# Kernel optimization log

Measured on AMD Instinct MI355X. Metric: run time of the kernel, lower is better.

The kernel has to match this reference:

```python
import jax, jax.numpy as jnp
import numpy as np

B, N, CIN, CK, M0 = 2, 4096, 64, 64, 64
NS = 16  # nsample; split into NS//2 cosine + NS//2 euclidean neighbors
LEAKY = 0.1


def _leaky(x):
    return jax.nn.leaky_relu(x, LEAKY)


def _knn_cosine(k, xyz, new_xyz):
    # xyz [B,M,C], new_xyz [B,S,C] -> idx [B,S,k] of smallest cosine distance
    s = new_xyz / jnp.sqrt(jnp.sum(new_xyz ** 2, -1, keepdims=True) + 1e-8)
    d = xyz / jnp.sqrt(jnp.sum(xyz ** 2, -1, keepdims=True) + 1e-8)
    dist = 1.0 - jnp.einsum('bsc,bmc->bsm', s, d)
    return jax.lax.top_k(-dist, k)[1]


def _knn_euclid(k, xyz, new_xyz):
    # squared euclidean distance [B,S,M]
    dist = (jnp.sum(new_xyz ** 2, -1)[:, :, None]
            + jnp.sum(xyz ** 2, -1)[:, None, :]
            - 2.0 * jnp.einsum('bsc,bmc->bsm', new_xyz, xyz))
    return jax.lax.top_k(-dist, k)[1]


def _group(points, idx):
    # points [B,M,C], idx [B,S,K] -> [B,S,K,C]
    return jax.vmap(lambda p, i: p[i])(points, idx)


def _cross(xyz1, xyz2, p1, p2, k1, k2, W_pos, b_pos, W_m1, b_m1, W_m2, b_m2):
    # all point tensors channel-first [B,C,N]; transpose to [B,N,C]
    xyz1t = xyz1.transpose(0, 2, 1)
    xyz2t = xyz2.transpose(0, 2, 1)
    p1t = p1.transpose(0, 2, 1)
    p2t = p2.transpose(0, 2, 1)
    k1t = k1.transpose(0, 2, 1)
    k2t = k2.transpose(0, 2, 1)
    kh = NS // 2
    idx_c = _knn_cosine(kh, k2t, k1t)      # [B,N1,kh] feature-space KNN
    idx_p = _knn_euclid(kh, xyz2t, xyz1t)  # [B,N1,kh] xyz-space KNN
    neighbor_xyz = jnp.concatenate([_group(xyz2t, idx_c), _group(xyz2t, idx_p)], axis=2)  # [B,N1,NS,3]
    direction = neighbor_xyz - xyz1t[:, :, None, :]
    g2 = jnp.concatenate([_group(p2t, idx_c), _group(p2t, idx_p)], axis=2)  # [B,N1,NS,D]
    pos = jnp.einsum('bnkc,dc->bnkd', direction, W_pos) + b_pos  # 1x1 conv on xyz offsets
    new = _leaky(g2 + p1t[:, :, None, :] + pos)  # fused add + leaky relu (bn=Identity)
    new = _leaky(jnp.einsum('bnkd,ed->bnke', new, W_m1) + b_m1)
    new = _leaky(jnp.einsum('bnkd,ed->bnke', new, W_m2) + b_m2)
    new = jnp.max(new, axis=2)  # max-pool over neighbor dim -> [B,N1,D]
    return new.transpose(0, 2, 1)  # [B,D,N1]


def setup_inputs() -> dict:
    key = jax.random.key(0)
    ks = jax.random.split(key, 12)
    rn = lambda k, shape, s=1.0: jax.random.normal(k, shape, jnp.float32) * s
    return {
        'pc1': rn(ks[0], (B, 3, N)),
        'pc2': rn(ks[1], (B, 3, N)),
        'feat1': rn(ks[2], (B, CIN, N)),
        'feat2': rn(ks[3], (B, CIN, N)),
        'knn1': rn(ks[4], (B, CK, N)),
        'knn2': rn(ks[5], (B, CK, N)),
        'W_t11': rn(ks[6], (M0, CIN), 0.1),
        'b_t11': jnp.zeros((M0,), jnp.float32),
        'W_t22': rn(ks[7], (M0, CIN), 0.1),
        'b_t22': jnp.zeros((M0,), jnp.float32),
        'W_pos': rn(ks[8], (M0, 3), 0.1),
        'b_pos': jnp.zeros((M0,), jnp.float32),
        'W_m1': rn(ks[9], (M0, M0), 0.1),
        'b_m1': jnp.zeros((M0,), jnp.float32),
        'W_m2': rn(ks[10], (M0, M0), 0.1),
        'b_m2': jnp.zeros((M0,), jnp.float32),
    }


def reference(pc1, pc2, feat1, feat2, knn1, knn2,
              W_t11, b_t11, W_t22, b_t22, W_pos, b_pos,
              W_m1, b_m1, W_m2, b_m2):
    # cross_t11 / cross_t22: 1x1 Conv1d in_channel -> mlp[0]
    f1a = jnp.einsum('dc,bcn->bdn', W_t11, feat1) + b_t11[None, :, None]
    f2a = jnp.einsum('dc,bcn->bdn', W_t22, feat2) + b_t22[None, :, None]
    f2b = jnp.einsum('dc,bcn->bdn', W_t11, feat2) + b_t11[None, :, None]
    f1b = jnp.einsum('dc,bcn->bdn', W_t22, feat1) + b_t22[None, :, None]
    feat1_new = _cross(pc1, pc2, f1a, f2a, knn1, knn2, W_pos, b_pos, W_m1, b_m1, W_m2, b_m2)
    feat2_new = _cross(pc2, pc1, f2b, f1b, knn2, knn1, W_pos, b_pos, W_m1, b_m1, W_m2, b_m2)
    return (feat1_new, feat2_new)
```

## Files before the change

### kernel.cpp

```cpp
#include <hip/hip_runtime.h>
#include <hip/hip_bf16.h>

#define BB 2
#define NN 4096
#define CH 64

typedef __bf16 bf16x8 __attribute__((ext_vector_type(8)));
typedef float f32x4 __attribute__((ext_vector_type(4)));

__device__ __forceinline__ float lrelu(float v) { return fmaxf(v, 0.1f * v); }
__device__ __forceinline__ float tobf(const __hip_bfloat16& h) { return __bfloat162float(h); }

#define PC1_C 0
#define PC2_C 24576
#define F1_C 49152
#define F2_C 573440
#define K1_C 1097728
#define K2_C 1622016
#define WT11_C 2146304
#define BT11_C 2150400
#define WT22_C 2150464
#define BT22_C 2154560
#define WPOS_C 2154624
#define BPOS_C 2154816
#define WM1_C 2154880
#define BM1_C 2158976
#define WM2_C 2159040
#define BM2_C 2163136
#define CN_TOTAL 2163200

__device__ __forceinline__ unsigned fmap(float s) {
  unsigned u = __float_as_uint(s);
  return u ^ ((unsigned)((int)u >> 31) | 0x80000000u);
}

__device__ __forceinline__ unsigned umaxu(unsigned a, unsigned b) { return a > b ? a : b; }
__device__ __forceinline__ void casu(unsigned& a, unsigned& b) {
  unsigned mx = a > b ? a : b;
  unsigned mn = a > b ? b : a;
  a = mx; b = mn;
}

__device__ __forceinline__ void bitonic8(unsigned bd[8]) {
  casu(bd[0], bd[4]); casu(bd[1], bd[5]); casu(bd[2], bd[6]); casu(bd[3], bd[7]);
  casu(bd[0], bd[2]); casu(bd[1], bd[3]); casu(bd[4], bd[6]); casu(bd[5], bd[7]);
  casu(bd[0], bd[1]); casu(bd[2], bd[3]); casu(bd[4], bd[5]); casu(bd[6], bd[7]);
}

__device__ __forceinline__ void merge4(unsigned bd[8], unsigned k0, unsigned k1,
                                       unsigned k2, unsigned k3) {
  casu(k0, k1); casu(k2, k3); casu(k0, k2); casu(k1, k3); casu(k1, k2);
  bd[4] = umaxu(bd[4], k3); bd[5] = umaxu(bd[5], k2);
  bd[6] = umaxu(bd[6], k1); bd[7] = umaxu(bd[7], k0);
  bitonic8(bd);
}

__device__ __forceinline__ void merge88(unsigned a[8], const unsigned b[8]) {
  a[0] = umaxu(a[0], b[7]); a[1] = umaxu(a[1], b[6]);
  a[2] = umaxu(a[2], b[5]); a[3] = umaxu(a[3], b[4]);
  a[4] = umaxu(a[4], b[3]); a[5] = umaxu(a[5], b[2]);
  a[6] = umaxu(a[6], b[1]); a[7] = umaxu(a[7], b[0]);
  bitonic8(a);
}

__global__ void k_detect(const unsigned short* __restrict__ pc1raw, int* __restrict__ flag) {
  int lane = threadIdx.x;
  int bad = 0;
#pragma unroll
  for (int i = 0; i < 64; ++i) {
    unsigned short u = pc1raw[lane * 64 + i];
    int e = (u >> 7) & 0xFF;
    bad += (e >= 140) ? 1 : 0;
  }
#pragma unroll
  for (int s = 32; s; s >>= 1) bad += __shfl_xor(bad, s, 64);
  if (lane == 0) *flag = (bad > 16) ? 1 : 0;
}

__global__ __launch_bounds__(256) void k_ingest(
    const void* p0, const void* p1, const void* p2, const void* p3,
    const void* p4, const void* p5, const void* p6, const void* p7,
    const void* p8, const void* p9, const void* p10, const void* p11,
    const void* p12, const void* p13, const void* p14, const void* p15,
    const int* __restrict__ flag, float* __restrict__ dst) {
  const int cum[17] = {0, 24576, 49152, 573440, 1097728, 1622016, 2146304, 2150400,
                       2150464, 2154560, 2154624, 2154816, 2154880, 2158976, 2159040,
                       2163136, 2163200};
  size_t t = (size_t)blockIdx.x * 256 + threadIdx.x;
  if (t >= (size_t)CN_TOTAL) return;
  int seg = 0;
#pragma unroll
  for (int i = 1; i < 16; ++i) seg += (t >= (size_t)cum[i]) ? 1 : 0;
  size_t local = t - (size_t)cum[seg];
  const void* ptrs[16] = {p0, p1, p2, p3, p4, p5, p6, p7, p8, p9, p10, p11, p12, p13, p14, p15};
  const void* p = ptrs[seg];
  float v;
  if (*flag) v = ((const float*)p)[local];
  else       v = tobf(((const __hip_bfloat16*)p)[local]);
  if (!(v == v) || fabsf(v) > 1e30f) v = 0.f;
  dst[t] = v;
}

__global__ __launch_bounds__(256) void k_prep_misc(const float* __restrict__ cn,
                                                   __hip_bfloat16* __restrict__ wmb,
                                                   float4* __restrict__ xyzt,
                                                   float4* __restrict__ wp4) {
  int bid = blockIdx.x;
  if (bid < 32) {
    int t = bid * 256 + threadIdx.x;
    float v = (t < 4096) ? cn[WM1_C + t] : cn[WM2_C + (t - 4096)];
    wmb[t] = __float2bfloat16(v);
  } else if (bid < 96) {
    int t = (bid - 32) * 256 + threadIdx.x;
    int n = t & (NN - 1);
    int b = (t >> 12) & 1;
    int a = t >> 13;
    const float* p = cn + (a ? PC2_C : PC1_C) + (size_t)b * 3 * NN + n;
    float x = p[0], y = p[NN], z = p[2 * NN];
    xyzt[(size_t)(a * BB + b) * NN + n] = make_float4(x, y, z, x * x + y * y + z * z);
  } else {
    int c = threadIdx.x;
    if (c < 64)
      wp4[c] = make_float4(cn[WPOS_C + 3 * c], cn[WPOS_C + 3 * c + 1],
                           cn[WPOS_C + 3 * c + 2], cn[BPOS_C + c]);
  }
}

__global__ __launch_bounds__(256) void k_prep_knn(const float* __restrict__ cn,
                                                  float* __restrict__ knnt,
                                                  __hip_bfloat16* __restrict__ knnb) {
  int t = blockIdx.x * 256 + threadIdx.x;
  int n = t & (NN - 1);
  int b = (t >> 12) & 1;
  int a = t >> 13;
  const float* col = cn + (a ? K2_C : K1_C) + (size_t)b * CH * NN + n;
  float s = 0.f;
#pragma unroll
  for (int c = 0; c < CH; ++c) { float v = col[(size_t)c * NN]; s += v * v; }
  float inv = 1.0f / sqrtf(s + 1e-8f);
  size_t row = (size_t)(a * BB + b) * NN + n;
  float* o = knnt + row * CH;
  __hip_bfloat16* ob = knnb + row * CH;
#pragma unroll
  for (int c = 0; c < CH; ++c) {
    float v = col[(size_t)c * NN] * inv;
    o[c] = v;
    ob[c] = __float2bfloat16(v);
  }
}

__global__ __launch_bounds__(256) void k_conv(const float* __restrict__ cn,
                                              float* __restrict__ fbuf) {
  __shared__ float wl[CH * CH];
  int bid = blockIdx.x;
  int tile = bid & (NN / 4 - 1);
  int b = (bid >> 10) & 1;
  int sel = bid >> 11;
  const float* W = cn + ((sel == 0 || sel == 2) ? WT11_C : WT22_C);
  const float* bias = cn + ((sel == 0 || sel == 2) ? BT11_C : BT22_C);
  const float* feat = cn + ((sel == 0 || sel == 3) ? F1_C : F2_C);
  int t = threadIdx.x;
#pragma unroll
  for (int i = 0; i < 16; ++i) {
    int e = t * 16 + i;
    wl[(e & 63) * 64 + (e >> 6)] = W[e];
  }
  __syncthreads();
  int p = t >> 6, d = t & 63;
  int n = tile * 4 + p;
  const float* fc = feat + (size_t)b * CH * NN + n;
  float acc = bias[d];
#pragma unroll
  for (int c = 0; c < CH; ++c) acc += wl[c * 64 + d] * fc[(size_t)c * NN];
  fbuf[((size_t)(sel * BB + b) * NN + n) * CH + d] = acc;
}

__global__ __launch_bounds__(512, 4) void k_knn3(const __hip_bfloat16* __restrict__ knnb,
                                                 const float* __restrict__ knnt,
                                                 const float4* __restrict__ xyzt,
                                                 int* __restrict__ idxf) {
  __shared__ unsigned skc[16 * 8 * 33];
  __shared__ unsigned ske[16 * 8 * 33];
  __shared__ int cidx[16 * 16];
  int bid = blockIdx.x;
  int qt = bid & (NN / 16 - 1);
  int b = (bid >> 8) & 1;
  int x = bid >> 9;
  int w = threadIdx.x >> 6;
  int lane = threadIdx.x & 63;
  int lo = lane & 15, g = lane >> 4;
  int q0 = qt * 16;
  int j0 = w * (NN / 8);
  int ss = w * 4 + g;
  int hw = lane >> 5, sl = lane & 31;
  int qq = w * 2 + hw;
  size_t qbase = (size_t)(x * BB + b) * NN;
  size_t dbase = (size_t)((1 - x) * BB + b) * NN;

  const __hip_bfloat16* qb = knnb + (qbase + q0) * CH;
  bf16x8 qf0 = *reinterpret_cast<const bf16x8*>(qb + lo * CH + g * 8);
  bf16x8 qf1 = *reinterpret_cast<const bf16x8*>(qb + lo * CH + 32 + g * 8);
  const __hip_bfloat16* db = knnb + dbase * CH;
  const float4 q4 = xyzt[qbase + q0 + lo];
  const float4* dbx = xyzt + dbase;
  float tx = 2.f * q4.x, ty = 2.f * q4.y, tz = 2.f * q4.z;

  unsigned bc0[8], bc1[8], be0[8], be1[8];
#pragma unroll
  for (int k = 0; k < 8; ++k) { bc0[k] = 0u; bc1[k] = 0u; be0[k] = 0u; be1[k] = 0u; }

  auto TILE = [&](unsigned (&bc)[8], unsigned (&be)[8], int jb) {
    unsigned rc = (unsigned)(4095 - jb - g * 4);
    const __hip_bfloat16* ar = db + (size_t)(jb + lo) * CH + g * 8;
    bf16x8 a0 = *reinterpret_cast<const bf16x8*>(ar);
    bf16x8 a1 = *reinterpret_cast<const bf16x8*>(ar + 32);
    f32x4 acc = {0.f, 0.f, 0.f, 0.f};
    acc = __builtin_amdgcn_mfma_f32_16x16x32_bf16(a0, qf0, acc, 0, 0, 0);
    acc = __builtin_amdgcn_mfma_f32_16x16x32_bf16(a1, qf1, acc, 0, 0, 0);
    int je = jb + g * 4;
    float4 p0 = dbx[je], p1 = dbx[je + 1], p2 = dbx[je + 2], p3 = dbx[je + 3];
    float v0 = fmaf(tx, p0.x, fmaf(ty, p0.y, fmaf(tz, p0.z, -p0.w)));
    float v1 = fmaf(tx, p1.x, fmaf(ty, p1.y, fmaf(tz, p1.z, -p1.w)));
    float v2 = fmaf(tx, p2.x, fmaf(ty, p2.y, fmaf(tz, p2.z, -p2.w)));
    float v3 = fmaf(tx, p3.x, fmaf(ty, p3.y, fmaf(tz, p3.z, -p3.w)));
    merge4(bc, (__float_as_uint(acc[0] + 4.0f) & 0xFFFFF000u) | rc,
               (__float_as_uint(acc[1] + 4.0f) & 0xFFFFF000u) | (rc - 1),
               (__float_as_uint(acc[2] + 4.0f) & 0xFFFFF000u) | (rc - 2),
               (__float_as_uint(acc[3] + 4.0f) & 0xFFFFF000u) | (rc - 3));
    merge4(be, (fmap(v0) & 0xFFFFF000u) | rc,
               (fmap(v1) & 0xFFFFF000u) | (rc - 1),
               (fmap(v2) & 0xFFFFF000u) | (rc - 2),
               (fmap(v3) & 0xFFFFF000u) | (rc - 3));
  };

  for (int t = 0; t < 16; ++t) {
    TILE(bc0, be0, j0 + (2 * t) * 16);
    TILE(bc1, be1, j0 + (2 * t + 1) * 16);
  }
  merge88(bc0, bc1);
  merge88(be0, be1);
#pragma unroll
  for (int k = 0; k < 8; ++k) {
    skc[(lo * 8 + k) * 33 + ss] = bc0[k];
    ske[(lo * 8 + k) * 33 + ss] = be0[k];
  }
  __syncthreads();

  {
    unsigned e[16];
#pragma unroll
    for (int k = 0; k < 8; ++k) e[k] = skc[(qq * 8 + k) * 33 + sl];
#pragma unroll
    for (int k = 8; k < 16; ++k) e[k] = 0u;
#pragma unroll
    for (int s = 1; s < 32; s <<= 1) {
      unsigned f[16];
#pragma unroll
      for (int k = 0; k < 16; ++k) f[k] = (unsigned)__shfl_xor((int)e[k], s, 64);
#pragma unroll
      for (int i = 0; i < 16; ++i) e[i] = umaxu(e[i], f[15 - i]);
      casu(e[0], e[8]); casu(e[1], e[9]); casu(e[2], e[10]); casu(e[3], e[11]);
      casu(e[4], e[12]); casu(e[5], e[13]); casu(e[6], e[14]); casu(e[7], e[15]);
      casu(e[0], e[4]); casu(e[1], e[5]); casu(e[2], e[6]); casu(e[3], e[7]);
      casu(e[8], e[12]); casu(e[9], e[13]); casu(e[10], e[14]); casu(e[11], e[15]);
      casu(e[0], e[2]); casu(e[1], e[3]); casu(e[4], e[6]); casu(e[5], e[7]);
      casu(e[8], e[10]); casu(e[9], e[11]); casu(e[12], e[14]); casu(e[13], e[15]);
      casu(e[0], e[1]); casu(e[2], e[3]); casu(e[4], e[5]); casu(e[6], e[7]);
      casu(e[8], e[9]); casu(e[10], e[11]); casu(e[12], e[13]); casu(e[14], e[15]);
    }
    if (sl == 0) {
#pragma unroll
      for (int k = 0; k < 16; ++k) cidx[qq * 16 + k] = 4095 - (int)(e[k] & 4095u);
    }
    int c = sl >> 1, hr = sl & 1;
    int idx = cidx[qq * 16 + c];
    const float4* qr = reinterpret_cast<const float4*>(knnt + (qbase + q0 + qq) * CH) + hr * 8;
    const float4* dr = reinterpret_cast<const float4*>(knnt + (dbase + idx) * CH) + hr * 8;
    float v = 0.f;
#pragma unroll 4
    for (int cb = 0; cb < 8; ++cb) {
      float4 qv = qr[cb], dv = dr[cb];
      v += qv.x * dv.x + qv.y * dv.y + qv.z * dv.z + qv.w * dv.w;
    }
    v += __shfl_xor(v, 1, 64);
    float cv = v; int ci = idx; int wsel = 0;
#pragma unroll
    for (int k = 0; k < 8; ++k) {
      float av = cv; int ai = ci;
#pragma unroll
      for (int s = 1; s < 32; s <<= 1) {
        float ov = __shfl_xor(av, s, 64);
        int oi = __shfl_xor(ai, s, 64);
        bool bt = (ov > av) || (ov == av && oi < ai);
        av = bt ? ov : av; ai = bt ? oi : ai;
      }
      if (sl == k) wsel = ai;
      if (ci == ai) cv = -1e38f;
    }
    if (sl < 8) idxf[(qbase + q0 + qq) * 16 + sl] = wsel;
  }

  {
    unsigned e[16];
#pragma unroll
    for (int k = 0; k < 8; ++k) e[k] = ske[(qq * 8 + k) * 33 + sl];
#pragma unroll
    for (int k = 8; k < 16; ++k) e[k] = 0u;
#pragma unroll
    for (int s = 1; s < 32; s <<= 1) {
      unsigned f[16];
#pragma unroll
      for (int k = 0; k < 16; ++k) f[k] = (unsigned)__shfl_xor((int)e[k], s, 64);
#pragma unroll
      for (int i = 0; i < 16; ++i) e[i] = umaxu(e[i], f[15 - i]);
      casu(e[0], e[8]); casu(e[1], e[9]); casu(e[2], e[10]); casu(e[3], e[11]);
      casu(e[4], e[12]); casu(e[5], e[13]); casu(e[6], e[14]); casu(e[7], e[15]);
      casu(e[0], e[4]); casu(e[1], e[5]); casu(e[2], e[6]); casu(e[3], e[7]);
      casu(e[8], e[12]); casu(e[9], e[13]); casu(e[10], e[14]); casu(e[11], e[15]);
      casu(e[0], e[2]); casu(e[1], e[3]); casu(e[4], e[6]); casu(e[5], e[7]);
      casu(e[8], e[10]); casu(e[9], e[11]); casu(e[12], e[14]); casu(e[13], e[15]);
      casu(e[0], e[1]); casu(e[2], e[3]); casu(e[4], e[5]); casu(e[6], e[7]);
      casu(e[8], e[9]); casu(e[10], e[11]); casu(e[12], e[13]); casu(e[14], e[15]);
    }
    if (sl == 0) {
#pragma unroll
      for (int k = 0; k < 16; ++k) cidx[qq * 16 + k] = 4095 - (int)(e[k] & 4095u);
    }
    int c = sl >> 1;
    int idx = cidx[qq * 16 + c];
    const float4 qx4 = xyzt[qbase + q0 + qq];
    float4 p = xyzt[dbase + idx];
    float v = fmaf(2.f * qx4.x, p.x, fmaf(2.f * qx4.y, p.y, fmaf(2.f * qx4.z, p.z, -p.w)));
    float cv = v; int ci = idx; int wsel = 0;
#pragma unroll
    for (int k = 0; k < 8; ++k) {
      float av = cv; int ai = ci;
#pragma unroll
      for (int s = 1; s < 32; s <<= 1) {
        float ov = __shfl_xor(av, s, 64);
        int oi = __shfl_xor(ai, s, 64);
        bool bt = (ov > av) || (ov == av && oi < ai);
        av = bt ? ov : av; ai = bt ? oi : ai;
      }
      if (sl == k) wsel = ai;
      if (ci == ai) cv = -1e38f;
    }
    if (sl < 8) idxf[(qbase + q0 + qq) * 16 + 8 + sl] = wsel;
  }
}

__global__ __launch_bounds__(256) void k_mlp(const float* __restrict__ fbuf,
                                             const float4* __restrict__ xyzt,
                                             const int* __restrict__ idxf,
                                             const float4* __restrict__ wp4,
                                             const __hip_bfloat16* __restrict__ wmb,
                                             const float* __restrict__ cn,
                                             float* __restrict__ out) {
  __shared__ __bf16 h1s[4 * 16 * 72];
  const int t = threadIdx.x;
  const int wv = t >> 6, L = t & 63;
  const int lo = L & 15, g = L >> 4;
  int bid = blockIdx.x;
  const int qt = bid & (NN / 4 - 1);
  const int b = (bid >> 10) & 1;
  const int x = bid >> 11;
  const int q = qt * 4 + wv;

  bf16x8 w1f[4][2], w2f[4][2];
#pragma unroll
  for (int tt = 0; tt < 4; ++tt)
#pragma unroll
    for (int kc = 0; kc < 2; ++kc) {
      int e = tt * 16 + lo, c0 = kc * 32 + g * 8;
      w1f[tt][kc] = *reinterpret_cast<const bf16x8*>(wmb + e * 64 + c0);
      w2f[tt][kc] = *reinterpret_cast<const bf16x8*>(wmb + 4096 + e * 64 + c0);
    }

  const float* pq  = fbuf + ((size_t)((x ? 2 : 0) * BB + b)) * NN * CH;
  const float* pdb = fbuf + ((size_t)((x ? 3 : 1) * BB + b)) * NN * CH;
  const float4* qx  = xyzt + (size_t)(x * BB + b) * NN;
  const float4* dbx = xyzt + (size_t)((1 - x) * BB + b) * NN;

  const int m = lo;
  int jm = idxf[(((size_t)x * BB + b) * NN + q) * 16 + m];
  jm &= (NN - 1);
  const float4 q4 = qx[q];
  const float4 p4 = dbx[jm];
  const float dx = p4.x - q4.x, dy = p4.y - q4.y, dz = p4.z - q4.z;

  const float4* g2v = reinterpret_cast<const float4*>(pdb + (size_t)jm * CH);
  const float4* pqv = reinterpret_cast<const float4*>(pq + (size_t)q * CH);
  float hv[16];
  {
    float4 t0 = g2v[g * 2], t1 = g2v[g * 2 + 1], t2 = g2v[g * 2 + 8], t3 = g2v[g * 2 + 9];
    float4 u0 = pqv[g * 2], u1 = pqv[g * 2 + 1], u2 = pqv[g * 2 + 8], u3 = pqv[g * 2 + 9];
    hv[0] = t0.x + u0.x; hv[1] = t0.y + u0.y; hv[2] = t0.z + u0.z; hv[3] = t0.w + u0.w;
    hv[4] = t1.x + u1.x; hv[5] = t1.y + u1.y; hv[6] = t1.z + u1.z; hv[7] = t1.w + u1.w;
    hv[8] = t2.x + u2.x; hv[9] = t2.y + u2.y; hv[10] = t2.z + u2.z; hv[11] = t2.w + u2.w;
    hv[12] = t3.x + u3.x; hv[13] = t3.y + u3.y; hv[14] = t3.z + u3.z; hv[15] = t3.w + u3.w;
  }

  bf16x8 a0, a1;
#pragma unroll
  for (int kc = 0; kc < 2; ++kc) {
#pragma unroll
    for (int j = 0; j < 8; ++j) {
      int c = kc * 32 + g * 8 + j;
      float4 wp = wp4[c];
      float v = hv[kc * 8 + j] + wp.x * dx + wp.y * dy + wp.z * dz + wp.w;
      v = lrelu(v);
      if (kc == 0) a0[j] = (__bf16)v; else a1[j] = (__bf16)v;
    }
  }

  __bf16* hrow = h1s + wv * 16 * 72;
#pragma unroll
  for (int tt = 0; tt < 4; ++tt) {
    float bv = cn[BM1_C + tt * 16 + lo];
    f32x4 acc = {bv, bv, bv, bv};
    acc = __builtin_amdgcn_mfma_f32_16x16x32_bf16(a0, w1f[tt][0], acc, 0, 0, 0);
    acc = __builtin_amdgcn_mfma_f32_16x16x32_bf16(a1, w1f[tt][1], acc, 0, 0, 0);
#pragma unroll
    for (int r = 0; r < 4; ++r) {
      float v = lrelu(acc[r]);
      hrow[(g * 4 + r) * 72 + tt * 16 + lo] = (__bf16)v;
    }
  }
  __syncthreads();
  bf16x8 h1a = *reinterpret_cast<const bf16x8*>(hrow + m * 72 + g * 8);
  bf16x8 h1b = *reinterpret_cast<const bf16x8*>(hrow + m * 72 + 32 + g * 8);

  size_t obase = ((size_t)(x * BB + b) * CH) * NN;
#pragma unroll
  for (int tt = 0; tt < 4; ++tt) {
    float bv = cn[BM2_C + tt * 16 + lo];
    f32x4 acc = {bv, bv, bv, bv};
    acc = __builtin_amdgcn_mfma_f32_16x16x32_bf16(h1a, w2f[tt][0], acc, 0, 0, 0);
    acc = __builtin_amdgcn_mfma_f32_16x16x32_bf16(h1b, w2f[tt][1], acc, 0, 0, 0);
    float v = fmaxf(fmaxf(lrelu(acc[0]), lrelu(acc[1])), fmaxf(lrelu(acc[2]), lrelu(acc[3])));
    v = fmaxf(v, __shfl_xor(v, 16, 64));
    v = fmaxf(v, __shfl_xor(v, 32, 64));
    if (g == 0) out[obase + (size_t)(tt * 16 + lo) * NN + q] = v;
  }
}

#define CN_OFF 0
#define FB_OFF ((size_t)CN_TOTAL)
#define KT_OFF (FB_OFF + (size_t)4 * BB * NN * CH)
#define XZ_OFF (KT_OFF + (size_t)2 * BB * NN * CH)
#define WP4_OFF (XZ_OFF + (size_t)2 * BB * NN * 4)
#define WMB_OFF (WP4_OFF + 256)
#define IDX_OFF (WMB_OFF + 4096)
#define FLAG_OFF (IDX_OFF + 262144)
#define KNB_OFF (FLAG_OFF + 4)

extern "C" void kernel_launch(void* const* d_in, const int* in_sizes, int n_in,
                              void* d_out, int out_size, void* d_ws, size_t ws_size,
                              hipStream_t stream) {
  float* ws = (float*)d_ws;
  float* cn = ws + CN_OFF;
  int* flag = (int*)(ws + FLAG_OFF);

  k_detect<<<1, 64, 0, stream>>>((const unsigned short*)d_in[0], flag);
  k_ingest<<<(CN_TOTAL + 255) / 256, 256, 0, stream>>>(
      d_in[0], d_in[1], d_in[2], d_in[3], d_in[4], d_in[5], d_in[6], d_in[7],
      d_in[8], d_in[9], d_in[10], d_in[11], d_in[12], d_in[13], d_in[14], d_in[15],
      flag, cn);
  k_prep_misc<<<97, 256, 0, stream>>>(cn, (__hip_bfloat16*)(ws + WMB_OFF),
                                      (float4*)(ws + XZ_OFF), (float4*)(ws + WP4_OFF));
  k_prep_knn<<<(2 * BB * NN) / 256, 256, 0, stream>>>(cn, ws + KT_OFF,
                                                     (__hip_bfloat16*)(ws + KNB_OFF));
  k_conv<<<4 * BB * (NN / 4), 256, 0, stream>>>(cn, ws + FB_OFF);
  k_knn3<<<2 * BB * (NN / 16), 512, 0, stream>>>(
      (const __hip_bfloat16*)(ws + KNB_OFF), ws + KT_OFF,
      (const float4*)(ws + XZ_OFF), (int*)(ws + IDX_OFF));
  k_mlp<<<2 * BB * (NN / 4), 256, 0, stream>>>(ws + FB_OFF, (const float4*)(ws + XZ_OFF),
                                               (const int*)(ws + IDX_OFF), (const float4*)(ws + WP4_OFF),
                                               (const __hip_bfloat16*)(ws + WMB_OFF), cn,
                                               (float*)d_out);
}
```

Baseline: 311.7 us.

## Prefetch KNN tiles, share one LDS buffer, use bitonic sort for rerank

The KNN kernel's main loop now software-pipelines its loads, issuing the bf16 feature and xyz loads for the next tile before the MFMA and merge work on the current tile. The cosine and euclidean candidate exchanges share a single LDS buffer with an extra barrier between them, halving that shared memory to help occupancy. The exact-distance refinement swaps eight serial argmax reductions for a bitonic sort across the 32 lanes. Risks include higher register pressure from holding two tiles of loads at once, and a change in tie-break order if the bitonic network differs from the old selection.

```diff
diff --git a/kernel.cpp b/kernel.cpp
--- a/kernel.cpp
+++ b/kernel.cpp
@@ -175,12 +175,11 @@
   fbuf[((size_t)(sel * BB + b) * NN + n) * CH + d] = acc;
 }
 
-__global__ __launch_bounds__(512, 4) void k_knn3(const __hip_bfloat16* __restrict__ knnb,
+__global__ __launch_bounds__(512, 4) void k_knn4(const __hip_bfloat16* __restrict__ knnb,
                                                  const float* __restrict__ knnt,
                                                  const float4* __restrict__ xyzt,
                                                  int* __restrict__ idxf) {
-  __shared__ unsigned skc[16 * 8 * 33];
-  __shared__ unsigned ske[16 * 8 * 33];
+  __shared__ unsigned sk[16 * 8 * 33];
   __shared__ int cidx[16 * 16];
   int bid = blockIdx.x;
   int qt = bid & (NN / 16 - 1);
@@ -209,47 +208,67 @@
 #pragma unroll
   for (int k = 0; k < 8; ++k) { bc0[k] = 0u; bc1[k] = 0u; be0[k] = 0u; be1[k] = 0u; }
 
-  auto TILE = [&](unsigned (&bc)[8], unsigned (&be)[8], int jb) {
-    unsigned rc = (unsigned)(4095 - jb - g * 4);
-    const __hip_bfloat16* ar = db + (size_t)(jb + lo) * CH + g * 8;
-    bf16x8 a0 = *reinterpret_cast<const bf16x8*>(ar);
-    bf16x8 a1 = *reinterpret_cast<const bf16x8*>(ar + 32);
+  auto STEP = [&](const bf16x8& A0, const bf16x8& A1, const float4& P0,
+                  const float4& P1, const float4& P2, const float4& P3,
+                  int rcv, unsigned (&bc)[8], unsigned (&be)[8]) {
     f32x4 acc = {0.f, 0.f, 0.f, 0.f};
-    acc = __builtin_amdgcn_mfma_f32_16x16x32_bf16(a0, qf0, acc, 0, 0, 0);
-    acc = __builtin_amdgcn_mfma_f32_16x16x32_bf16(a1, qf1, acc, 0, 0, 0);
-    int je = jb + g * 4;
-    float4 p0 = dbx[je], p1 = dbx[je + 1], p2 = dbx[je + 2], p3 = dbx[je + 3];
-    float v0 = fmaf(tx, p0.x, fmaf(ty, p0.y, fmaf(tz, p0.z, -p0.w)));
-    float v1 = fmaf(tx, p1.x, fmaf(ty, p1.y, fmaf(tz, p1.z, -p1.w)));
-    float v2 = fmaf(tx, p2.x, fmaf(ty, p2.y, fmaf(tz, p2.z, -p2.w)));
-    float v3 = fmaf(tx, p3.x, fmaf(ty, p3.y, fmaf(tz, p3.z, -p3.w)));
-    merge4(bc, (__float_as_uint(acc[0] + 4.0f) & 0xFFFFF000u) | rc,
-               (__float_as_uint(acc[1] + 4.0f) & 0xFFFFF000u) | (rc - 1),
-               (__float_as_uint(acc[2] + 4.0f) & 0xFFFFF000u) | (rc - 2),
-               (__float_as_uint(acc[3] + 4.0f) & 0xFFFFF000u) | (rc - 3));
-    merge4(be, (fmap(v0) & 0xFFFFF000u) | rc,
-               (fmap(v1) & 0xFFFFF000u) | (rc - 1),
-               (fmap(v2) & 0xFFFFF000u) | (rc - 2),
-               (fmap(v3) & 0xFFFFF000u) | (rc - 3));
+    acc = __builtin_amdgcn_mfma_f32_16x16x32_bf16(A0, qf0, acc, 0, 0, 0);
+    acc = __builtin_amdgcn_mfma_f32_16x16x32_bf16(A1, qf1, acc, 0, 0, 0);
+    float v0 = fmaf(tx, P0.x, fmaf(ty, P0.y, fmaf(tz, P0.z, -P0.w)));
+    float v1 = fmaf(tx, P1.x, fmaf(ty, P1.y, fmaf(tz, P1.z, -P1.w)));
+    float v2 = fmaf(tx, P2.x, fmaf(ty, P2.y, fmaf(tz, P2.z, -P2.w)));
+    float v3 = fmaf(tx, P3.x, fmaf(ty, P3.y, fmaf(tz, P3.z, -P3.w)));
+    unsigned r = (unsigned)rcv;
+    merge4(bc, (__float_as_uint(acc[0] + 4.0f) & 0xFFFFF000u) | r,
+               (__float_as_uint(acc[1] + 4.0f) & 0xFFFFF000u) | (r - 1),
+               (__float_as_uint(acc[2] + 4.0f) & 0xFFFFF000u) | (r - 2),
+               (__float_as_uint(acc[3] + 4.0f) & 0xFFFFF000u) | (r - 3));
+    merge4(be, (fmap(v0) & 0xFFFFF000u) | r,
+               (fmap(v1) & 0xFFFFF000u) | (r - 1),
+               (fmap(v2) & 0xFFFFF000u) | (r - 2),
+               (fmap(v3) & 0xFFFFF000u) | (r - 3));
   };
 
-  for (int t = 0; t < 16; ++t) {
-    TILE(bc0, be0, j0 + (2 * t) * 16);
-    TILE(bc1, be1, j0 + (2 * t + 1) * 16);
+  const __hip_bfloat16* arA = db + (size_t)(j0 + lo) * CH + g * 8;
+  const __hip_bfloat16* arB = arA + 16 * CH;
+  const float4* peA = dbx + j0 + g * 4;
+  const float4* peB = peA + 16;
+  int rc = 4095 - j0 - g * 4;
+
+  bf16x8 aA0 = *reinterpret_cast<const bf16x8*>(arA);
+  bf16x8 aA1 = *reinterpret_cast<const bf16x8*>(arA + 32);
+  float4 pA0 = peA[0], pA1 = peA[1], pA2 = peA[2], pA3 = peA[3];
+
+  for (int i = 0; i < 15; ++i) {
+    bf16x8 aB0 = *reinterpret_cast<const bf16x8*>(arB);
+    bf16x8 aB1 = *reinterpret_cast<const bf16x8*>(arB + 32);
+    float4 pB0 = peB[0], pB1 = peB[1], pB2 = peB[2], pB3 = peB[3];
+    STEP(aA0, aA1, pA0, pA1, pA2, pA3, rc, bc0, be0);
+    arA += 32 * CH; peA += 32;
+    aA0 = *reinterpret_cast<const bf16x8*>(arA);
+    aA1 = *reinterpret_cast<const bf16x8*>(arA + 32);
+    pA0 = peA[0]; pA1 = peA[1]; pA2 = peA[2]; pA3 = peA[3];
+    STEP(aB0, aB1, pB0, pB1, pB2, pB3, rc - 16, bc1, be1);
+    arB += 32 * CH; peB += 32;
+    rc -= 32;
+  }
+  {
+    bf16x8 aB0 = *reinterpret_cast<const bf16x8*>(arB);
+    bf16x8 aB1 = *reinterpret_cast<const bf16x8*>(arB + 32);
+    float4 pB0 = peB[0], pB1 = peB[1], pB2 = peB[2], pB3 = peB[3];
+    STEP(aA0, aA1, pA0, pA1, pA2, pA3, rc, bc0, be0);
+    STEP(aB0, aB1, pB0, pB1, pB2, pB3, rc - 16, bc1, be1);
   }
   merge88(bc0, bc1);
   merge88(be0, be1);
-#pragma unroll
-  for (int k = 0; k < 8; ++k) {
-    skc[(lo * 8 + k) * 33 + ss] = bc0[k];
-    ske[(lo * 8 + k) * 33 + ss] = be0[k];
-  }
+
+#pragma unroll
+  for (int k = 0; k < 8; ++k) sk[(lo * 8 + k) * 33 + ss] = bc0[k];
   __syncthreads();
-
   {
     unsigned e[16];
 #pragma unroll
-    for (int k = 0; k < 8; ++k) e[k] = skc[(qq * 8 + k) * 33 + sl];
+    for (int k = 0; k < 8; ++k) e[k] = sk[(qq * 8 + k) * 33 + sl];
 #pragma unroll
     for (int k = 8; k < 16; ++k) e[k] = 0u;
 #pragma unroll
@@ -283,27 +302,31 @@
       v += qv.x * dv.x + qv.y * dv.y + qv.z * dv.z + qv.w * dv.w;
     }
     v += __shfl_xor(v, 1, 64);
-    float cv = v; int ci = idx; int wsel = 0;
-#pragma unroll
-    for (int k = 0; k < 8; ++k) {
-      float av = cv; int ai = ci;
-#pragma unroll
-      for (int s = 1; s < 32; s <<= 1) {
-        float ov = __shfl_xor(av, s, 64);
-        int oi = __shfl_xor(ai, s, 64);
-        bool bt = (ov > av) || (ov == av && oi < ai);
-        av = bt ? ov : av; ai = bt ? oi : ai;
+    int ii = idx;
+#pragma unroll
+    for (int k = 2; k <= 32; k <<= 1) {
+#pragma unroll
+      for (int j = k >> 1; j >= 1; j >>= 1) {
+        float ov = __shfl_xor(v, j, 64);
+        int oi = __shfl_xor(ii, j, 64);
+        bool ob = (ov > v) || (ov == v && oi < ii);
+        bool want = (((sl & k) == 0) == ((sl & j) == 0));
+        bool take = (want == ob);
+        v = take ? ov : v;
+        ii = take ? oi : ii;
       }
-      if (sl == k) wsel = ai;
-      if (ci == ai) cv = -1e38f;
-    }
-    if (sl < 8) idxf[(qbase + q0 + qq) * 16 + sl] = wsel;
-  }
-
+    }
+    if (sl < 16 && (sl & 1) == 0) idxf[(qbase + q0 + qq) * 16 + (sl >> 1)] = ii;
+  }
+  __syncthreads();
+
+#pragma unroll
+  for (int k = 0; k < 8; ++k) sk[(lo * 8 + k) * 33 + ss] = be0[k];
+  __syncthreads();
   {
     unsigned e[16];
 #pragma unroll
-    for (int k = 0; k < 8; ++k) e[k] = ske[(qq * 8 + k) * 33 + sl];
+    for (int k = 0; k < 8; ++k) e[k] = sk[(qq * 8 + k) * 33 + sl];
 #pragma unroll
     for (int k = 8; k < 16; ++k) e[k] = 0u;
 #pragma unroll
@@ -331,21 +354,21 @@
     const float4 qx4 = xyzt[qbase + q0 + qq];
     float4 p = xyzt[dbase + idx];
     float v = fmaf(2.f * qx4.x, p.x, fmaf(2.f * qx4.y, p.y, fmaf(2.f * qx4.z, p.z, -p.w)));
-    float cv = v; int ci = idx; int wsel = 0;
-#pragma unroll
-    for (int k = 0; k < 8; ++k) {
-      float av = cv; int ai = ci;
-#pragma unroll
-      for (int s = 1; s < 32; s <<= 1) {
-        float ov = __shfl_xor(av, s, 64);
-        int oi = __shfl_xor(ai, s, 64);
-        bool bt = (ov > av) || (ov == av && oi < ai);
-        av = bt ? ov : av; ai = bt ? oi : ai;
+    int ii = idx;
+#pragma unroll
+    for (int k = 2; k <= 32; k <<= 1) {
+#pragma unroll
+      for (int j = k >> 1; j >= 1; j >>= 1) {
+        float ov = __shfl_xor(v, j, 64);
+        int oi = __shfl_xor(ii, j, 64);
+        bool ob = (ov > v) || (ov == v && oi < ii);
+        bool want = (((sl & k) == 0) == ((sl & j) == 0));
+        bool take = (want == ob);
+        v = take ? ov : v;
+        ii = take ? oi : ii;
       }
-      if (sl == k) wsel = ai;
-      if (ci == ai) cv = -1e38f;
-    }
-    if (sl < 8) idxf[(qbase + q0 + qq) * 16 + 8 + sl] = wsel;
+    }
+    if (sl < 16 && (sl & 1) == 0) idxf[(qbase + q0 + qq) * 16 + 8 + (sl >> 1)] = ii;
   }
 }
 
@@ -471,7 +494,7 @@
   k_prep_knn<<<(2 * BB * NN) / 256, 256, 0, stream>>>(cn, ws + KT_OFF,
                                                      (__hip_bfloat16*)(ws + KNB_OFF));
   k_conv<<<4 * BB * (NN / 4), 256, 0, stream>>>(cn, ws + FB_OFF);
-  k_knn3<<<2 * BB * (NN / 16), 512, 0, stream>>>(
+  k_knn4<<<2 * BB * (NN / 16), 512, 0, stream>>>(
       (const __hip_bfloat16*)(ws + KNB_OFF), ws + KT_OFF,
       (const float4*)(ws + XZ_OFF), (int*)(ws + IDX_OFF));
   k_mlp<<<2 * BB * (NN / 4), 256, 0, stream>>>(ws + FB_OFF, (const float4*)(ws + XZ_OFF),
```

New measurement: 304.4 us. -2.3%, faster.
